# Performance work log

Measured on AMD Instinct MI355X. Metric: run time of the kernel, lower is better.

Reference implementation:

```python
import jax, jax.numpy as jnp
import numpy as np

N_NODES = 100000
N_EDGES = 1600000
F_IN, F_HID, F_OUT = 64, 64, 32


def setup_inputs() -> dict:
    key = jax.random.key(0)
    k1, k2, k3, k4 = jax.random.split(key, 4)
    x = jax.random.normal(k1, (N_NODES, F_IN), dtype=jnp.float32)
    edge_idx = jax.random.randint(k2, (2, N_EDGES), 0, N_NODES, dtype=jnp.int64)
    W1 = jax.random.normal(k3, (F_IN, F_HID), dtype=jnp.float32) * (1.0 / np.sqrt(F_IN))
    b1 = jnp.zeros((F_HID,), dtype=jnp.float32)
    W2 = jax.random.normal(k4, (F_HID, F_OUT), dtype=jnp.float32) * (1.0 / np.sqrt(F_HID))
    b2 = jnp.zeros((F_OUT,), dtype=jnp.float32)
    return {"x": x, "edge_idx": edge_idx, "W1": W1, "b1": b1, "W2": W2, "b2": b2}


def _gcn_conv(h, src, dst, norm, W, b, n):
    # PyG GCNConv: transform first, then normalized sum aggregation, then bias.
    h = h @ W                                   # [N, F_out]
    msg = h[src] * norm[:, None]                # [E+N, F_out] gather + scale
    agg = jax.ops.segment_sum(msg, dst, num_segments=n)  # scatter-add
    return agg + b


def reference(x, edge_idx, W1, b1, W2, b2):
    n = x.shape[0]
    loop = jnp.arange(n, dtype=edge_idx.dtype)
    src = jnp.concatenate([edge_idx[0], loop])  # add self-loops
    dst = jnp.concatenate([edge_idx[1], loop])
    # symmetric normalization D^-1/2 (A+I) D^-1/2
    deg = jax.ops.segment_sum(jnp.ones_like(dst, dtype=x.dtype), dst, num_segments=n)
    dinv = jnp.where(deg > 0, jax.lax.rsqrt(deg), 0.0)
    norm = dinv[src] * dinv[dst]                # [E+N]

    h = _gcn_conv(x, src, dst, norm, W1, b1, n)
    h = jax.nn.relu(h)
    # dropout(p=0.5) is identity in eval mode (deterministic reference)
    out = _gcn_conv(h, src, dst, norm, W2, b2, n)
    return out
```

## Files before the change

kernel.cpp:

```cpp
#include <hip/hip_runtime.h>
#include <hip/hip_bf16.h>
#include <hip/hip_fp16.h>


#define N_FEAT_IN 64
#define B2SHIFT 9
#define CHUNK 4096
#define CAP 12288
#define CSRCAP 16384

struct alignas(8) half4 { __half2 lo, hi; };
struct alignas(16) half8 { __half2 h[4]; };

__global__ __launch_bounds__(256) void init_k(int* __restrict__ gcur) {
    gcur[threadIdx.x] = 0;
}

__global__ __launch_bounds__(1024) void place_k(const int* __restrict__ src,
                                                const int* __restrict__ dst,
                                                int* __restrict__ gcur,
                                                unsigned* __restrict__ bedges, int E) {
    __shared__ int h[256];
    __shared__ int cur[256];
    int t = threadIdx.x;
    if (t < 256) h[t] = 0;
    __syncthreads();
    int base = blockIdx.x * CHUNK;
    int end = min(base + CHUNK, E);
    for (int i = base + t; i < end; i += 1024)
        atomicAdd(&h[dst[i] >> B2SHIFT], 1);
    __syncthreads();
    if (t < 256) {
        int cnt = h[t];
        int b0 = cnt ? atomicAdd(&gcur[t], cnt) : 0;
        cur[t] = t * CAP + b0;
    }
    __syncthreads();
    for (int i = base + t; i < end; i += 1024) {
        int d = dst[i];
        int p = atomicAdd(&cur[d >> B2SHIFT], 1);
        bedges[p] = ((unsigned)src[i] << B2SHIFT) | (unsigned)(d & 511);
    }
}

__global__ __launch_bounds__(1024) void bucket_csr(const int* __restrict__ gcnt,
                                                   const unsigned* __restrict__ bedges,
                                                   int* __restrict__ row_ptr,
                                                   int* __restrict__ rend,
                                                   float* __restrict__ dinv,
                                                   int* __restrict__ csr_src, int n) {
    __shared__ int lh[512];
    __shared__ int cur[512];
    int t = threadIdx.x;
    if (t < 512) lh[t] = 0;
    __syncthreads();
    int b = blockIdx.x;
    int beg = b * CAP;
    int end = beg + gcnt[b];
    for (int i = beg + t; i < end; i += 1024)
        atomicAdd(&lh[bedges[i] & 511], 1);
    __syncthreads();
    int c = (t < 512) ? lh[t] : 0;
    __syncthreads();
    int cp = (c + 7) & ~7;
    if (t < 512) lh[t] = cp;
    __syncthreads();
    for (int off = 1; off < 512; off <<= 1) {
        int a = (t < 512 && t >= off) ? lh[t - off] : 0;
        __syncthreads();
        if (t < 512) lh[t] += a;
        __syncthreads();
    }
    int pb = b * CSRCAP;
    if (t < 512) {
        int d = (b << B2SHIFT) + t;
        int rbeg = pb + lh[t] - cp;
        cur[t] = rbeg;
        if (d < n) {
            row_ptr[d] = rbeg;
            rend[d] = rbeg + cp;
            dinv[d] = rsqrtf((float)c + 1.0f);
            for (int i = c; i < cp; ++i) csr_src[rbeg + i] = n;
        }
    }
    __syncthreads();
    for (int i = beg + t; i < end; i += 1024) {
        unsigned v = bedges[i];
        int p = atomicAdd(&cur[v & 511], 1);
        csr_src[p] = (int)(v >> B2SHIFT);
    }
}

__global__ __launch_bounds__(256) void gemm64(const float* __restrict__ A,
                                              const float* __restrict__ W,
                                              const float* __restrict__ dinv,
                                              __half* __restrict__ outh, int n) {
    __shared__ float AsT[64][132];
    __shared__ float Ws[64][64];

    const int t = threadIdx.x;
    const int r0 = blockIdx.x * 128;

    if (blockIdx.x == 0 && t < 64)
        outh[(size_t)n * 64 + t] = __float2half(0.f);

    for (int i = t; i < 64 * 16; i += 256) {
        int k = i >> 4;
        int c4 = (i & 15) * 4;
        *(float4*)&Ws[k][c4] = *(const float4*)&W[k * 64 + c4];
    }
    for (int i = t; i < 128 * 16; i += 256) {
        int row = i >> 4;
        int c4 = (i & 15) * 4;
        int g = r0 + row;
        float4 v = make_float4(0.f, 0.f, 0.f, 0.f);
        if (g < n) v = *(const float4*)&A[(size_t)g * 64 + c4];
        AsT[c4 + 0][row] = v.x;
        AsT[c4 + 1][row] = v.y;
        AsT[c4 + 2][row] = v.z;
        AsT[c4 + 3][row] = v.w;
    }
    __syncthreads();

    const int rg = t >> 3;
    const int cg = t & 7;
    float acc[4][8];
#pragma unroll
    for (int r = 0; r < 4; ++r)
#pragma unroll
        for (int j = 0; j < 8; ++j) acc[r][j] = 0.f;

#pragma unroll 4
    for (int k = 0; k < 64; ++k) {
        float4 a = *(const float4*)&AsT[k][rg * 4];
        float4 w0 = *(const float4*)&Ws[k][cg * 8];
        float4 w1 = *(const float4*)&Ws[k][cg * 8 + 4];
        float av[4] = {a.x, a.y, a.z, a.w};
        float wv[8] = {w0.x, w0.y, w0.z, w0.w, w1.x, w1.y, w1.z, w1.w};
#pragma unroll
        for (int r = 0; r < 4; ++r)
#pragma unroll
            for (int j = 0; j < 8; ++j)
                acc[r][j] = fmaf(av[r], wv[j], acc[r][j]);
    }

#pragma unroll
    for (int r = 0; r < 4; ++r) {
        int g = r0 + rg * 4 + r;
        if (g < n) {
            float sc = dinv[g];
            half8 h;
            h.h[0] = __floats2half2_rn(acc[r][0] * sc, acc[r][1] * sc);
            h.h[1] = __floats2half2_rn(acc[r][2] * sc, acc[r][3] * sc);
            h.h[2] = __floats2half2_rn(acc[r][4] * sc, acc[r][5] * sc);
            h.h[3] = __floats2half2_rn(acc[r][6] * sc, acc[r][7] * sc);
            *(half8*)&outh[(size_t)g * 64 + cg * 8] = h;
        }
    }
}

#define ACC8(v)                                                       \
    {                                                                 \
        float2 f0 = __half22float2((v).h[0]);                         \
        float2 f1 = __half22float2((v).h[1]);                         \
        float2 f2 = __half22float2((v).h[2]);                         \
        float2 f3 = __half22float2((v).h[3]);                         \
        a0 += f0.x; a1 += f0.y; a2 += f1.x; a3 += f1.y;               \
        a4 += f2.x; a5 += f2.y; a6 += f3.x; a7 += f3.y;               \
    }

__global__ __launch_bounds__(256) void agg64(const int* __restrict__ row_ptr,
                                             const int* __restrict__ rend,
                                             const int* __restrict__ csr_src,
                                             const float* __restrict__ dinv,
                                             const __half* __restrict__ xs1,
                                             const float* __restrict__ b1,
                                             __half* __restrict__ th, int n) {
    int d = blockIdx.x * 32 + (threadIdx.x >> 3);
    if (d >= n) return;
    int c = threadIdx.x & 7;
    const half8* __restrict__ xrow = (const half8*)xs1 + c;

    half8 sv = xrow[(size_t)d * 8];
    float a0, a1, a2, a3, a4, a5, a6, a7;
    {
        float2 f0 = __half22float2(sv.h[0]), f1 = __half22float2(sv.h[1]);
        float2 f2 = __half22float2(sv.h[2]), f3 = __half22float2(sv.h[3]);
        a0 = f0.x; a1 = f0.y; a2 = f1.x; a3 = f1.y;
        a4 = f2.x; a5 = f2.y; a6 = f3.x; a7 = f3.y;
    }

    int beg = row_ptr[d];
    int end = rend[d];
    if (beg < end) {
        int4 ia = *(const int4*)&csr_src[beg];
        int4 ib = *(const int4*)&csr_src[beg + 4];
        int jb = beg;
        for (;;) {
            int jn = jb + 8;
            bool more = jn < end;
            int js = more ? jn : beg;
            int4 na = *(const int4*)&csr_src[js];
            int4 nb = *(const int4*)&csr_src[js + 4];
            half8 v0 = xrow[(size_t)ia.x * 8];
            half8 v1 = xrow[(size_t)ia.y * 8];
            half8 v2 = xrow[(size_t)ia.z * 8];
            half8 v3 = xrow[(size_t)ia.w * 8];
            half8 v4 = xrow[(size_t)ib.x * 8];
            half8 v5 = xrow[(size_t)ib.y * 8];
            half8 v6 = xrow[(size_t)ib.z * 8];
            half8 v7 = xrow[(size_t)ib.w * 8];
            ACC8(v0); ACC8(v1); ACC8(v2); ACC8(v3);
            ACC8(v4); ACC8(v5); ACC8(v6); ACC8(v7);
            if (!more) break;
            jb = jn; ia = na; ib = nb;
        }
    }

    float di = dinv[d];
    float4 ba = *(const float4*)&b1[8 * c];
    float4 bb = *(const float4*)&b1[8 * c + 4];
    float t0 = fmaxf(fmaf(di, a0, ba.x), 0.f);
    float t1 = fmaxf(fmaf(di, a1, ba.y), 0.f);
    float t2 = fmaxf(fmaf(di, a2, ba.z), 0.f);
    float t3 = fmaxf(fmaf(di, a3, ba.w), 0.f);
    float t4 = fmaxf(fmaf(di, a4, bb.x), 0.f);
    float t5 = fmaxf(fmaf(di, a5, bb.y), 0.f);
    float t6 = fmaxf(fmaf(di, a6, bb.z), 0.f);
    float t7 = fmaxf(fmaf(di, a7, bb.w), 0.f);
    half8 o;
    o.h[0] = __floats2half2_rn(t0, t1);
    o.h[1] = __floats2half2_rn(t2, t3);
    o.h[2] = __floats2half2_rn(t4, t5);
    o.h[3] = __floats2half2_rn(t6, t7);
    *(half8*)&th[(size_t)d * 64 + 8 * c] = o;
}

__global__ __launch_bounds__(256) void gemm32h(const __half* __restrict__ Ah,
                                               const float* __restrict__ W,
                                               const float* __restrict__ dinv,
                                               __half* __restrict__ outh, int n) {
    __shared__ float AsT[64][260];
    __shared__ float Ws[64][32];

    const int t = threadIdx.x;
    const int r0 = blockIdx.x * 256;

    if (blockIdx.x == 0 && t < 32)
        outh[(size_t)n * 32 + t] = __float2half(0.f);

    for (int i = t; i < 64 * 8; i += 256) {
        int k = i >> 3;
        int c4 = (i & 7) * 4;
        *(float4*)&Ws[k][c4] = *(const float4*)&W[k * 32 + c4];
    }
    for (int i = t; i < 256 * 8; i += 256) {
        int row = i >> 3;
        int c8 = (i & 7) * 8;
        int g = r0 + row;
        if (g < n) {
            half8 hv = *(const half8*)&Ah[(size_t)g * 64 + c8];
            float2 f0 = __half22float2(hv.h[0]), f1 = __half22float2(hv.h[1]);
            float2 f2 = __half22float2(hv.h[2]), f3 = __half22float2(hv.h[3]);
            AsT[c8 + 0][row] = f0.x; AsT[c8 + 1][row] = f0.y;
            AsT[c8 + 2][row] = f1.x; AsT[c8 + 3][row] = f1.y;
            AsT[c8 + 4][row] = f2.x; AsT[c8 + 5][row] = f2.y;
            AsT[c8 + 6][row] = f3.x; AsT[c8 + 7][row] = f3.y;
        } else {
#pragma unroll
            for (int j = 0; j < 8; ++j) AsT[c8 + j][row] = 0.f;
        }
    }
    __syncthreads();

    const int rg = t >> 2;
    const int cg = t & 3;
    float acc[4][8];
#pragma unroll
    for (int r = 0; r < 4; ++r)
#pragma unroll
        for (int j = 0; j < 8; ++j) acc[r][j] = 0.f;

#pragma unroll 4
    for (int k = 0; k < 64; ++k) {
        float4 a = *(const float4*)&AsT[k][rg * 4];
        float4 w0 = *(const float4*)&Ws[k][cg * 8];
        float4 w1 = *(const float4*)&Ws[k][cg * 8 + 4];
        float av[4] = {a.x, a.y, a.z, a.w};
        float wv[8] = {w0.x, w0.y, w0.z, w0.w, w1.x, w1.y, w1.z, w1.w};
#pragma unroll
        for (int r = 0; r < 4; ++r)
#pragma unroll
            for (int j = 0; j < 8; ++j)
                acc[r][j] = fmaf(av[r], wv[j], acc[r][j]);
    }

#pragma unroll
    for (int r = 0; r < 4; ++r) {
        int g = r0 + rg * 4 + r;
        if (g < n) {
            float sc = dinv[g];
            half8 h;
            h.h[0] = __floats2half2_rn(acc[r][0] * sc, acc[r][1] * sc);
            h.h[1] = __floats2half2_rn(acc[r][2] * sc, acc[r][3] * sc);
            h.h[2] = __floats2half2_rn(acc[r][4] * sc, acc[r][5] * sc);
            h.h[3] = __floats2half2_rn(acc[r][6] * sc, acc[r][7] * sc);
            *(half8*)&outh[(size_t)g * 32 + cg * 8] = h;
        }
    }
}

__global__ __launch_bounds__(256) void agg32(const int* __restrict__ row_ptr,
                                             const int* __restrict__ rend,
                                             const int* __restrict__ csr_src,
                                             const float* __restrict__ dinv,
                                             const __half* __restrict__ xs2,
                                             const float* __restrict__ b2,
                                             float* __restrict__ out, int n) {
    int d = blockIdx.x * 64 + (threadIdx.x >> 2);
    if (d >= n) return;
    int c = threadIdx.x & 3;
    const half8* __restrict__ xrow = (const half8*)xs2 + c;

    half8 sv = xrow[(size_t)d * 4];
    float a0, a1, a2, a3, a4, a5, a6, a7;
    {
        float2 f0 = __half22float2(sv.h[0]), f1 = __half22float2(sv.h[1]);
        float2 f2 = __half22float2(sv.h[2]), f3 = __half22float2(sv.h[3]);
        a0 = f0.x; a1 = f0.y; a2 = f1.x; a3 = f1.y;
        a4 = f2.x; a5 = f2.y; a6 = f3.x; a7 = f3.y;
    }

    int beg = row_ptr[d];
    int end = rend[d];
    if (beg < end) {
        int4 ia = *(const int4*)&csr_src[beg];
        int4 ib = *(const int4*)&csr_src[beg + 4];
        int jb = beg;
        for (;;) {
            int jn = jb + 8;
            bool more = jn < end;
            int js = more ? jn : beg;
            int4 na = *(const int4*)&csr_src[js];
            int4 nb = *(const int4*)&csr_src[js + 4];
            half8 v0 = xrow[(size_t)ia.x * 4];
            half8 v1 = xrow[(size_t)ia.y * 4];
            half8 v2 = xrow[(size_t)ia.z * 4];
            half8 v3 = xrow[(size_t)ia.w * 4];
            half8 v4 = xrow[(size_t)ib.x * 4];
            half8 v5 = xrow[(size_t)ib.y * 4];
            half8 v6 = xrow[(size_t)ib.z * 4];
            half8 v7 = xrow[(size_t)ib.w * 4];
            ACC8(v0); ACC8(v1); ACC8(v2); ACC8(v3);
            ACC8(v4); ACC8(v5); ACC8(v6); ACC8(v7);
            if (!more) break;
            jb = jn; ia = na; ib = nb;
        }
    }

    float di = dinv[d];
    float4 ba = *(const float4*)&b2[8 * c];
    float4 bb = *(const float4*)&b2[8 * c + 4];
    float4 r0, r1;
    r0.x = fmaf(di, a0, ba.x);
    r0.y = fmaf(di, a1, ba.y);
    r0.z = fmaf(di, a2, ba.z);
    r0.w = fmaf(di, a3, ba.w);
    r1.x = fmaf(di, a4, bb.x);
    r1.y = fmaf(di, a5, bb.y);
    r1.z = fmaf(di, a6, bb.z);
    r1.w = fmaf(di, a7, bb.w);
    *(float4*)&out[(size_t)d * 32 + 8 * c] = r0;
    *(float4*)&out[(size_t)d * 32 + 8 * c + 4] = r1;
}

extern "C" void kernel_launch(void* const* d_in, const int* in_sizes, int n_in,
                              void* d_out, int out_size, void* d_ws, size_t ws_size,
                              hipStream_t stream) {
    const float* x  = (const float*)d_in[0];
    const int*   ei = (const int*)d_in[1];
    const float* W1 = (const float*)d_in[2];
    const float* b1 = (const float*)d_in[3];
    const float* W2 = (const float*)d_in[4];
    const float* b2 = (const float*)d_in[5];
    float* out = (float*)d_out;

    const int n = in_sizes[0] / N_FEAT_IN;
    const int E = in_sizes[1] / 2;
    const int* srcI = ei;
    const int* dstI = ei + E;

    const int NB = (n + 511) >> B2SHIFT;
    const int NR = (E + CHUNK - 1) / CHUNK;

    char* ws = (char*)d_ws;
    size_t off = 0;
    auto alloc = [&](size_t bytes) {
        void* p = ws + off;
        off += (bytes + 255) & ~(size_t)255;
        return p;
    };
    float*    dinv    = (float*)alloc((size_t)n * 4);
    int*      row_ptr = (int*)alloc((size_t)(n + 1) * 4);
    int*      rend    = (int*)alloc((size_t)n * 4);
    int*      gcur    = (int*)alloc((size_t)256 * 4);
    unsigned* bedges  = (unsigned*)alloc((size_t)NB * CAP * 4);
    int*      csr_src = (int*)alloc((size_t)NB * CSRCAP * 4);
    __half*   xs1     = (__half*)alloc((size_t)(n + 1) * 64 * 2);
    __half*   th      = (__half*)alloc((size_t)n * 64 * 2);
    __half*   xs2     = (__half*)alloc((size_t)(n + 1) * 32 * 2);

    init_k<<<1, 256, 0, stream>>>(gcur);
    place_k<<<NR, 1024, 0, stream>>>(srcI, dstI, gcur, bedges, E);
    bucket_csr<<<NB, 1024, 0, stream>>>(gcur, bedges, row_ptr, rend, dinv, csr_src, n);

    gemm64<<<(n + 127) / 128, 256, 0, stream>>>(x, W1, dinv, xs1, n);

    agg64<<<(n + 31) / 32, 256, 0, stream>>>(row_ptr, rend, csr_src, dinv, xs1, b1, th, n);

    gemm32h<<<(n + 255) / 256, 256, 0, stream>>>(th, W2, dinv, xs2, n);

    agg32<<<(n + 63) / 64, 256, 0, stream>>>(row_ptr, rend, csr_src, dinv, xs2, b2, out, n);
}
```

Measured before the change: 198.5 us.

## Partition CSR neighbor lists into four source-range slices per destination

Each destination's neighbor list is split into four sub-lists keyed by the high bits of the source index, each padded to a multiple of eight. Per-node row ranges become int4 start/end pairs, and both aggregation kernels loop over the four slices. The intent is better cache locality of feature-row gathers by grouping sources by address range. The cost is much more padding work on low-degree nodes and more per-node loop overhead.

```diff
diff --git a/kernel.cpp b/kernel.cpp
--- a/kernel.cpp
+++ b/kernel.cpp
@@ -7,7 +7,8 @@
 #define B2SHIFT 9
 #define CHUNK 4096
 #define CAP 12288
-#define CSRCAP 16384
+#define CSRCAP 26624
+#define SSHIFT 15
 
 struct alignas(8) half4 { __half2 lo, hi; };
 struct alignas(16) half8 { __half2 h[4]; };
@@ -45,48 +46,71 @@
 
 __global__ __launch_bounds__(1024) void bucket_csr(const int* __restrict__ gcnt,
                                                    const unsigned* __restrict__ bedges,
-                                                   int* __restrict__ row_ptr,
-                                                   int* __restrict__ rend,
+                                                   int4* __restrict__ rp4,
+                                                   int4* __restrict__ re4,
                                                    float* __restrict__ dinv,
                                                    int* __restrict__ csr_src, int n) {
-    __shared__ int lh[512];
-    __shared__ int cur[512];
+    __shared__ int lh[2048];
+    __shared__ int cur[2048];
     int t = threadIdx.x;
-    if (t < 512) lh[t] = 0;
+    lh[t] = 0; lh[t + 1024] = 0;
     __syncthreads();
     int b = blockIdx.x;
     int beg = b * CAP;
     int end = beg + gcnt[b];
-    for (int i = beg + t; i < end; i += 1024)
-        atomicAdd(&lh[bedges[i] & 511], 1);
-    __syncthreads();
-    int c = (t < 512) ? lh[t] : 0;
-    __syncthreads();
-    int cp = (c + 7) & ~7;
-    if (t < 512) lh[t] = cp;
-    __syncthreads();
-    for (int off = 1; off < 512; off <<= 1) {
-        int a = (t < 512 && t >= off) ? lh[t - off] : 0;
+    for (int i = beg + t; i < end; i += 1024) {
+        unsigned v = bedges[i];
+        atomicAdd(&lh[(v & 511) * 4 + (v >> (B2SHIFT + SSHIFT))], 1);
+    }
+    __syncthreads();
+    int raw[4], pad[4];
+    if (t < 512) {
+#pragma unroll
+        for (int s = 0; s < 4; ++s) {
+            raw[s] = lh[t * 4 + s];
+            pad[s] = (raw[s] + 7) & ~7;
+        }
+    }
+    __syncthreads();
+    if (t < 512) {
+#pragma unroll
+        for (int s = 0; s < 4; ++s) lh[t * 4 + s] = pad[s];
+    }
+    __syncthreads();
+    for (int off = 1; off < 2048; off <<= 1) {
+        int a0 = (t >= off) ? lh[t - off] : 0;
+        int a1 = (t + 1024 >= off) ? lh[t + 1024 - off] : 0;
         __syncthreads();
-        if (t < 512) lh[t] += a;
+        lh[t] += a0;
+        lh[t + 1024] += a1;
         __syncthreads();
     }
     int pb = b * CSRCAP;
     if (t < 512) {
         int d = (b << B2SHIFT) + t;
-        int rbeg = pb + lh[t] - cp;
-        cur[t] = rbeg;
+        int e[4];
+#pragma unroll
+        for (int s = 0; s < 4; ++s) e[s] = lh[t * 4 + s] - pad[s];
+#pragma unroll
+        for (int s = 0; s < 4; ++s) cur[t * 4 + s] = pb + e[s];
         if (d < n) {
-            row_ptr[d] = rbeg;
-            rend[d] = rbeg + cp;
+            int4 rp = make_int4(pb + e[0], pb + e[1], pb + e[2], pb + e[3]);
+            int4 re = make_int4(pb + e[0] + pad[0], pb + e[1] + pad[1],
+                                pb + e[2] + pad[2], pb + e[3] + pad[3]);
+            rp4[d] = rp;
+            re4[d] = re;
+            int c = raw[0] + raw[1] + raw[2] + raw[3];
             dinv[d] = rsqrtf((float)c + 1.0f);
-            for (int i = c; i < cp; ++i) csr_src[rbeg + i] = n;
+#pragma unroll
+            for (int s = 0; s < 4; ++s)
+                for (int i = raw[s]; i < pad[s]; ++i)
+                    csr_src[pb + e[s] + i] = n;
         }
     }
     __syncthreads();
     for (int i = beg + t; i < end; i += 1024) {
         unsigned v = bedges[i];
-        int p = atomicAdd(&cur[v & 511], 1);
+        int p = atomicAdd(&cur[(v & 511) * 4 + (v >> (B2SHIFT + SSHIFT))], 1);
         csr_src[p] = (int)(v >> B2SHIFT);
     }
 }
@@ -169,8 +193,37 @@
         a4 += f2.x; a5 += f2.y; a6 += f3.x; a7 += f3.y;               \
     }
 
-__global__ __launch_bounds__(256) void agg64(const int* __restrict__ row_ptr,
-                                             const int* __restrict__ rend,
+#define AGG_SLICE_LOOP(STRIDE)                                        \
+    for (int s = 0; s < 4; ++s) {                                     \
+        int beg = rps[s];                                             \
+        int end = res[s];                                             \
+        if (beg >= end) continue;                                     \
+        int4 ia = *(const int4*)&csr_src[beg];                        \
+        int4 ib = *(const int4*)&csr_src[beg + 4];                    \
+        int jb = beg;                                                 \
+        for (;;) {                                                    \
+            int jn = jb + 8;                                          \
+            bool more = jn < end;                                     \
+            int js = more ? jn : beg;                                 \
+            int4 na = *(const int4*)&csr_src[js];                     \
+            int4 nb = *(const int4*)&csr_src[js + 4];                 \
+            half8 v0 = xrow[(size_t)ia.x * STRIDE];                   \
+            half8 v1 = xrow[(size_t)ia.y * STRIDE];                   \
+            half8 v2 = xrow[(size_t)ia.z * STRIDE];                   \
+            half8 v3 = xrow[(size_t)ia.w * STRIDE];                   \
+            half8 v4 = xrow[(size_t)ib.x * STRIDE];                   \
+            half8 v5 = xrow[(size_t)ib.y * STRIDE];                   \
+            half8 v6 = xrow[(size_t)ib.z * STRIDE];                   \
+            half8 v7 = xrow[(size_t)ib.w * STRIDE];                   \
+            ACC8(v0); ACC8(v1); ACC8(v2); ACC8(v3);                   \
+            ACC8(v4); ACC8(v5); ACC8(v6); ACC8(v7);                   \
+            if (!more) break;                                         \
+            jb = jn; ia = na; ib = nb;                                \
+        }                                                             \
+    }
+
+__global__ __launch_bounds__(256) void agg64(const int4* __restrict__ rp4,
+                                             const int4* __restrict__ re4,
                                              const int* __restrict__ csr_src,
                                              const float* __restrict__ dinv,
                                              const __half* __restrict__ xs1,
@@ -190,32 +243,11 @@
         a4 = f2.x; a5 = f2.y; a6 = f3.x; a7 = f3.y;
     }
 
-    int beg = row_ptr[d];
-    int end = rend[d];
-    if (beg < end) {
-        int4 ia = *(const int4*)&csr_src[beg];
-        int4 ib = *(const int4*)&csr_src[beg + 4];
-        int jb = beg;
-        for (;;) {
-            int jn = jb + 8;
-            bool more = jn < end;
-            int js = more ? jn : beg;
-            int4 na = *(const int4*)&csr_src[js];
-            int4 nb = *(const int4*)&csr_src[js + 4];
-            half8 v0 = xrow[(size_t)ia.x * 8];
-            half8 v1 = xrow[(size_t)ia.y * 8];
-            half8 v2 = xrow[(size_t)ia.z * 8];
-            half8 v3 = xrow[(size_t)ia.w * 8];
-            half8 v4 = xrow[(size_t)ib.x * 8];
-            half8 v5 = xrow[(size_t)ib.y * 8];
-            half8 v6 = xrow[(size_t)ib.z * 8];
-            half8 v7 = xrow[(size_t)ib.w * 8];
-            ACC8(v0); ACC8(v1); ACC8(v2); ACC8(v3);
-            ACC8(v4); ACC8(v5); ACC8(v6); ACC8(v7);
-            if (!more) break;
-            jb = jn; ia = na; ib = nb;
-        }
-    }
+    int4 rp = rp4[d];
+    int4 re = re4[d];
+    int rps[4] = {rp.x, rp.y, rp.z, rp.w};
+    int res[4] = {re.x, re.y, re.z, re.w};
+    AGG_SLICE_LOOP(8)
 
     float di = dinv[d];
     float4 ba = *(const float4*)&b1[8 * c];
@@ -310,8 +342,8 @@
     }
 }
 
-__global__ __launch_bounds__(256) void agg32(const int* __restrict__ row_ptr,
-                                             const int* __restrict__ rend,
+__global__ __launch_bounds__(256) void agg32(const int4* __restrict__ rp4,
+                                             const int4* __restrict__ re4,
                                              const int* __restrict__ csr_src,
                                              const float* __restrict__ dinv,
                                              const __half* __restrict__ xs2,
@@ -331,32 +363,11 @@
         a4 = f2.x; a5 = f2.y; a6 = f3.x; a7 = f3.y;
     }
 
-    int beg = row_ptr[d];
-    int end = rend[d];
-    if (beg < end) {
-        int4 ia = *(const int4*)&csr_src[beg];
-        int4 ib = *(const int4*)&csr_src[beg + 4];
-        int jb = beg;
-        for (;;) {
-            int jn = jb + 8;
-            bool more = jn < end;
-            int js = more ? jn : beg;
-            int4 na = *(const int4*)&csr_src[js];
-            int4 nb = *(const int4*)&csr_src[js + 4];
-            half8 v0 = xrow[(size_t)ia.x * 4];
-            half8 v1 = xrow[(size_t)ia.y * 4];
-            half8 v2 = xrow[(size_t)ia.z * 4];
-            half8 v3 = xrow[(size_t)ia.w * 4];
-            half8 v4 = xrow[(size_t)ib.x * 4];
-            half8 v5 = xrow[(size_t)ib.y * 4];
-            half8 v6 = xrow[(size_t)ib.z * 4];
-            half8 v7 = xrow[(size_t)ib.w * 4];
-            ACC8(v0); ACC8(v1); ACC8(v2); ACC8(v3);
-            ACC8(v4); ACC8(v5); ACC8(v6); ACC8(v7);
-            if (!more) break;
-            jb = jn; ia = na; ib = nb;
-        }
-    }
+    int4 rp = rp4[d];
+    int4 re = re4[d];
+    int rps[4] = {rp.x, rp.y, rp.z, rp.w};
+    int res[4] = {re.x, re.y, re.z, re.w};
+    AGG_SLICE_LOOP(4)
 
     float di = dinv[d];
     float4 ba = *(const float4*)&b2[8 * c];
@@ -401,8 +412,8 @@
         return p;
     };
     float*    dinv    = (float*)alloc((size_t)n * 4);
-    int*      row_ptr = (int*)alloc((size_t)(n + 1) * 4);
-    int*      rend    = (int*)alloc((size_t)n * 4);
+    int4*     rp4     = (int4*)alloc((size_t)n * 16);
+    int4*     re4     = (int4*)alloc((size_t)n * 16);
     int*      gcur    = (int*)alloc((size_t)256 * 4);
     unsigned* bedges  = (unsigned*)alloc((size_t)NB * CAP * 4);
     int*      csr_src = (int*)alloc((size_t)NB * CSRCAP * 4);
@@ -412,13 +423,13 @@
 
     init_k<<<1, 256, 0, stream>>>(gcur);
     place_k<<<NR, 1024, 0, stream>>>(srcI, dstI, gcur, bedges, E);
-    bucket_csr<<<NB, 1024, 0, stream>>>(gcur, bedges, row_ptr, rend, dinv, csr_src, n);
+    bucket_csr<<<NB, 1024, 0, stream>>>(gcur, bedges, rp4, re4, dinv, csr_src, n);
 
     gemm64<<<(n + 127) / 128, 256, 0, stream>>>(x, W1, dinv, xs1, n);
 
-    agg64<<<(n + 31) / 32, 256, 0, stream>>>(row_ptr, rend, csr_src, dinv, xs1, b1, th, n);
+    agg64<<<(n + 31) / 32, 256, 0, stream>>>(rp4, re4, csr_src, dinv, xs1, b1, th, n);
 
     gemm32h<<<(n + 255) / 256, 256, 0, stream>>>(th, W2, dinv, xs2, n);
 
-    agg32<<<(n + 63) / 64, 256, 0, stream>>>(row_ptr, rend, csr_src, dinv, xs2, b2, out, n);
-}
+    agg32<<<(n + 63) / 64, 256, 0, stream>>>(rp4, re4, csr_src, dinv, xs2, b2, out, n);
+}
```

Result: slower. 209.8 us (+5.7%).
